# Performance work log

Hardware: AMD Instinct MI355X
Metric: run time of the kernel (lower is better)

## Reference

```python
import jax, jax.numpy as jnp
from jax import lax
import numpy as np

NHEADS = 8

def _conv_block2d(x, w, b):
    y = lax.conv_general_dilated(x, w, (2, 2), [(1, 1), (1, 1)],
                                 dimension_numbers=('NCHW', 'OIHW', 'NCHW'))
    return jax.nn.gelu(y + b[None, :, None, None])

def _conv_block3d(x, w, b):
    y = lax.conv_general_dilated(x, w, (2, 2, 2), [(1, 1)] * 3,
                                 dimension_numbers=('NCDHW', 'OIDHW', 'NCDHW'))
    return jax.nn.gelu(y + b[None, :, None, None, None])

def _layernorm(x, g, b, eps=1e-5):
    mu = x.mean(-1, keepdims=True)
    var = x.var(-1, keepdims=True)
    return (x - mu) / jnp.sqrt(var + eps) * g + b

def _neighborhood_attn(x, g, bln, qkv_w, qkv_b, proj_w, proj_b, dw=5, hw=7, ww=7):
    # x: [B, C, D, H, W]; 3D neighborhood attention, window (dw,hw,ww), zero-pad + mask
    B, C, D, H, W = x.shape
    h, hd = NHEADS, C // NHEADS
    xt = jnp.transpose(x, (0, 2, 3, 4, 1))               # [B,D,H,W,C]
    y = _layernorm(xt, g, bln)
    qkv = y @ qkv_w + qkv_b                               # [B,D,H,W,3C]
    qkv = qkv.reshape(B, D, H, W, 3, h, hd)
    qkv = jnp.transpose(qkv, (4, 0, 5, 6, 1, 2, 3))       # [3,B,h,hd,D,H,W]
    q, k, v = qkv[0] * (hd ** -0.5), qkv[1], qkv[2]
    pz, py, px = dw // 2, hw // 2, ww // 2
    pad = ((0, 0), (0, 0), (0, 0), (pz, pz), (py, py), (px, px))
    kp, vp = jnp.pad(k, pad), jnp.pad(v, pad)
    valid = jnp.pad(jnp.ones((D, H, W), x.dtype), ((pz, pz), (py, py), (px, px)))
    offs = jnp.stack(jnp.meshgrid(jnp.arange(dw), jnp.arange(hw), jnp.arange(ww), indexing='ij'), -1).reshape(-1, 3)

    def score_step(_, o):
        ks = lax.dynamic_slice(kp, (0, 0, 0, o[0], o[1], o[2]), (B, h, hd, D, H, W))
        m = lax.dynamic_slice(valid, (o[0], o[1], o[2]), (D, H, W))
        return None, ((q * ks).sum(2), m)

    _, (scores, masks) = lax.scan(score_step, None, offs)  # [245,B,h,D,H,W],[245,D,H,W]
    neg = jnp.finfo(scores.dtype).min
    scores = jnp.where(masks[:, None, None] > 0, scores, neg)
    probs = jax.nn.softmax(scores, axis=0)

    def out_step(acc, xs):
        o, p = xs
        vs = lax.dynamic_slice(vp, (0, 0, 0, o[0], o[1], o[2]), (B, h, hd, D, H, W))
        return acc + p[:, :, None] * vs, None

    out0 = jnp.zeros((B, h, hd, D, H, W), x.dtype)
    out, _ = lax.scan(out_step, out0, (offs, probs))
    out = jnp.transpose(out, (0, 3, 4, 5, 1, 2)).reshape(B, D, H, W, C)
    out = out @ proj_w + proj_b
    return x + jnp.transpose(out, (0, 4, 1, 2, 3))

def setup_inputs() -> dict:
    key = jax.random.key(0)
    ks = jax.random.split(key, 16)
    rn = lambda i, shp, s: jax.random.normal(ks[i], shp, jnp.float32) * s
    return {
        'x_2d': rn(0, (1, 8, 256, 512), 1.0),
        'x_3d': rn(1, (1, 5, 24, 256, 512), 1.0),
        'sw0': rn(2, (128, 8, 3, 3), 0.02), 'sb0': jnp.zeros((128,), jnp.float32),
        'sw1': rn(3, (256, 128, 3, 3), 0.02), 'sb1': jnp.zeros((256,), jnp.float32),
        'sw2': rn(4, (512, 256, 3, 3), 0.02), 'sb2': jnp.zeros((512,), jnp.float32),
        'pw0': rn(5, (128, 5, 3, 3, 3), 0.02), 'pb0': jnp.zeros((128,), jnp.float32),
        'pw1': rn(6, (256, 128, 3, 3, 3), 0.02), 'pb1': jnp.zeros((256,), jnp.float32),
        'pw2': rn(7, (512, 256, 3, 3, 3), 0.02), 'pb2': jnp.zeros((512,), jnp.float32),
        'lat_w': rn(8, (512, 512, 1, 1, 1), 0.02), 'lat_b': jnp.zeros((512,), jnp.float32),
        'ln_g': jnp.ones((3, 512), jnp.float32), 'ln_b': jnp.zeros((3, 512), jnp.float32),
        'qkv_w': rn(9, (3, 512, 1536), 0.02), 'qkv_b': jnp.zeros((3, 1536), jnp.float32),
        'proj_w': rn(10, (3, 512, 512), 0.02), 'proj_b': jnp.zeros((3, 512), jnp.float32),
    }

def reference(x_2d, x_3d, sw0, sb0, sw1, sb1, sw2, sb2,
              pw0, pb0, pw1, pb1, pw2, pb2, lat_w, lat_b,
              ln_g, ln_b, qkv_w, qkv_b, proj_w, proj_b):
    s = x_2d
    for w_, b_ in ((sw0, sb0), (sw1, sb1), (sw2, sb2)):
        s = _conv_block2d(s, w_, b_)
    p = x_3d
    for w_, b_ in ((pw0, pb0), (pw1, pb1), (pw2, pb2)):
        p = _conv_block3d(p, w_, b_)
    feats = jnp.concatenate([p, s[:, :, None]], axis=2)   # [B,512,D/8+1,H/8,W/8]
    lat = lax.conv_general_dilated(feats, lat_w, (1, 1, 1), 'VALID',
                                   dimension_numbers=('NCDHW', 'OIDHW', 'NCDHW'))
    lat = lat + lat_b[None, :, None, None, None]
    for i in range(3):
        lat = _neighborhood_attn(lat, ln_g[i], ln_b[i], qkv_w[i], qkv_b[i], proj_w[i], proj_b[i])
    return lat
```

## Files before the change

kernel.cpp:

```cpp
#include <hip/hip_runtime.h>
#include <hip/hip_bf16.h>
#include <math.h>

typedef __hip_bfloat16 bf16;
typedef __attribute__((ext_vector_type(8))) short s8v;
typedef __attribute__((ext_vector_type(4))) float f4v;

__device__ __forceinline__ float ldf(const float* p) { return *p; }
__device__ __forceinline__ float ldf(const bf16* p) { return __bfloat162float(*p); }
__device__ __forceinline__ void stf(float* p, float v) { *p = v; }
__device__ __forceinline__ void stf(bf16* p, float v) { *p = __float2bfloat16(v); }

__device__ __forceinline__ float gelu_tanh(float x) {
    float x3 = x * x * x;
    return 0.5f * x * (1.f + tanhf(0.7978845608028654f * (x + 0.044715f * x3)));
}
__device__ __forceinline__ unsigned short bfbits(float x) {
    bf16 t = __float2bfloat16(x);
    return *(unsigned short*)&t;
}

__device__ __forceinline__ void gload16(const bf16* g, bf16* l)
{
    __builtin_amdgcn_global_load_lds(
        (const __attribute__((address_space(1))) unsigned int*)g,
        (__attribute__((address_space(3))) unsigned int*)l,
        16, 0, 0);
}

__global__ __launch_bounds__(256) void fillcol_k(uint4* __restrict__ p, int nrows,
                                                 int strideGran, int granPerRow)
{
    int i = blockIdx.x * 256 + threadIdx.x;
    int row = i / granPerRow, g = i - row * granPerRow;
    if (row < nrows) p[(size_t)row * strideGran + g] = uint4{0u, 0u, 0u, 0u};
}

__global__ __launch_bounds__(256) void tcast_k(const float* __restrict__ in,
                                               bf16* __restrict__ out, int R, int C)
{
    __shared__ float t[64][65];
    int r0 = blockIdx.x * 64, c0 = blockIdx.y * 64;
    for (int i = threadIdx.x; i < 4096; i += 256) {
        int rr = i >> 6, cc = i & 63;
        int r = r0 + rr, c = c0 + cc;
        t[rr][cc] = (c < C) ? in[(size_t)r * C + c] : 0.f;
    }
    __syncthreads();
    for (int i = threadIdx.x; i < 4096; i += 256) {
        int cc = i >> 6, rr = i & 63;
        int r = r0 + rr, c = c0 + cc;
        if (c < C)
            out[(size_t)c * R + r] = __float2bfloat16(t[rr][cc]);
    }
}

__global__ __launch_bounds__(256) void w1prep_k(const float* __restrict__ w, bf16* __restrict__ o,
                                                int OC, int nic, int ntap, int Kp)
{
    int i = blockIdx.x * 256 + threadIdx.x;
    if (i >= OC * Kp) return;
    int oc = i / Kp, k = i - oc * Kp;
    float v = 0.f;
    if (k < nic * ntap) {
        int tap = k / nic, ic = k - tap * nic;
        v = w[((size_t)oc * nic + ic) * ntap + tap];
    }
    o[i] = __float2bfloat16(v);
}

__global__ __launch_bounds__(256) void cast_k(const float* __restrict__ w, bf16* __restrict__ o, int n)
{
    int i = blockIdx.x * 256 + threadIdx.x;
    if (i < n) o[i] = __float2bfloat16(w[i]);
}

__global__ __launch_bounds__(256) void im2col3d_k(const float* __restrict__ x, bf16* __restrict__ A, int od0)
{
    int gid = blockIdx.x * 256 + threadIdx.x;
    int m = gid / 20, kg = gid - 20 * (gid / 20);
    int ow = m & 255, rowid = m >> 8;
    int oh = rowid & 127, od = od0 + (rowid >> 7);
    int iz0 = 2 * od - 1, iy0 = 2 * oh - 1, ix0 = 2 * ow - 1;
    union { uint4 u; unsigned short h[8]; } pk;
#pragma unroll
    for (int j = 0; j < 8; j++) {
        int k = kg * 8 + j;
        float v = 0.f;
        if (k < 135) {
            int tap = k / 5, ic = k - tap * 5;
            int kz = tap / 9, r = tap - kz * 9;
            int ky = r / 3, kx = r - ky * 3;
            int iz = iz0 + kz, iy = iy0 + ky, ix = ix0 + kx;
            if ((unsigned)iz < 24u && (unsigned)iy < 256u && (unsigned)ix < 512u)
                v = x[(((size_t)ic * 24 + iz) * 256 + iy) * 512 + ix];
        }
        pk.h[j] = bfbits(v);
    }
    *(uint4*)&A[(size_t)m * 160 + kg * 8] = pk.u;
}

__global__ __launch_bounds__(256) void im2col2d_k(const float* __restrict__ x, bf16* __restrict__ A)
{
    int gid = blockIdx.x * 256 + threadIdx.x;
    int m = gid / 12, kg = gid - 12 * (gid / 12);
    int ow = m & 255, oh = m >> 8;
    int iy0 = 2 * oh - 1, ix0 = 2 * ow - 1;
    union { uint4 u; unsigned short h[8]; } pk;
#pragma unroll
    for (int j = 0; j < 8; j++) {
        int k = kg * 8 + j;
        float v = 0.f;
        if (k < 72) {
            int tap = k >> 3, ic = k & 7;
            int ky = tap / 3, kx = tap - ky * 3;
            int iy = iy0 + ky, ix = ix0 + kx;
            if ((unsigned)iy < 256u && (unsigned)ix < 512u)
                v = x[((size_t)ic * 256 + iy) * 512 + ix];
        }
        pk.h[j] = bfbits(v);
    }
    *(uint4*)&A[(size_t)m * 96 + kg * 8] = pk.u;
}

__global__ __launch_bounds__(256) void conv1_gemm(
    const bf16* __restrict__ A, const bf16* __restrict__ W, const float* __restrict__ bias,
    bf16* __restrict__ out, int M, int Kp, int rowOff)
{
    __shared__ __align__(16) bf16 As[128 * 32];
    __shared__ __align__(16) bf16 Bs[128 * 32];
    int tid = threadIdx.x;
    int m0 = blockIdx.x * 128;
    int wave = tid >> 6, lane = tid & 63;
    int wb = tid & 192;
    int wm = (wave >> 1) * 64, wn = (wave & 1) * 64;
    int lm = lane & 15, lq = lane >> 4;
    f4v acc[4][4];
#pragma unroll
    for (int i = 0; i < 4; i++)
#pragma unroll
        for (int j = 0; j < 4; j++) acc[i][j] = f4v{0.f, 0.f, 0.f, 0.f};
    for (int k0 = 0; k0 < Kp; k0 += 32) {
        __syncthreads();
#pragma unroll
        for (int c = 0; c < 2; c++) {
            int i = c * 256 + tid;
            int row = i >> 2, kq = i & 3;
            gload16(&A[(size_t)(m0 + row) * Kp + k0 + kq * 8], &As[(c * 256 + wb) * 8]);
            gload16(&W[(size_t)row * Kp + k0 + kq * 8], &Bs[(c * 256 + wb) * 8]);
        }
        __syncthreads();
        s8v af[4], bfr[4];
#pragma unroll
        for (int mi = 0; mi < 4; mi++) af[mi] = *(const s8v*)&As[(wm + mi * 16 + lm) * 32 + lq * 8];
#pragma unroll
        for (int ni = 0; ni < 4; ni++) bfr[ni] = *(const s8v*)&Bs[(wn + ni * 16 + lm) * 32 + lq * 8];
#pragma unroll
        for (int mi = 0; mi < 4; mi++)
#pragma unroll
            for (int ni = 0; ni < 4; ni++)
                acc[mi][ni] = __builtin_amdgcn_mfma_f32_16x16x32_bf16(af[mi], bfr[ni], acc[mi][ni], 0, 0, 0);
    }
#pragma unroll
    for (int mi = 0; mi < 4; mi++)
#pragma unroll
        for (int ni = 0; ni < 4; ni++)
#pragma unroll
            for (int r = 0; r < 4; r++) {
                int m = m0 + wm + mi * 16 + lq * 4 + r;
                int n = wn + ni * 16 + lm;
                int row = rowOff + (m >> 8), x = m & 255;
                float v = acc[mi][ni][r] + bias[n];
                out[((size_t)row * 258 + 1 + x) * 128 + n] = __float2bfloat16(gelu_tanh(v));
            }
}

template <int BM, int KD>
__global__ __launch_bounds__(256) void conv_mfma2(
    const bf16* __restrict__ in, const bf16* __restrict__ wr, const float* __restrict__ bias,
    bf16* __restrict__ out, int ID, int IH, int IWp, int IC,
    int OH, int OC, int OWS, int outPad, int nx)
{
    constexpr int NI = (BM == 128) ? 4 : 2;
    __shared__ __align__(16) bf16 As[3 * BM * 32];
    __shared__ __align__(16) bf16 Bs[3 * 128 * 32];
    int tid = threadIdx.x;
    int nwg = gridDim.x;
    int bl = blockIdx.x;
    int swz = (bl & 7) * (nwg >> 3) + (bl >> 3);
    int n0 = (swz % nx) * 128;
    int rowid = swz / nx;
    int od = rowid / OH, oh = rowid % OH;
    int wave = tid >> 6, lane = tid & 63;
    int wb = tid & 192;
    int wm = (BM == 128) ? (wave >> 1) * 64 : 0;
    int wn = (BM == 128) ? (wave & 1) * 64 : wave * 32;
    int lm = lane & 15, lq = lane >> 4;
    f4v acc[4][NI];
#pragma unroll
    for (int i = 0; i < 4; i++)
#pragma unroll
        for (int j = 0; j < NI; j++) acc[i][j] = f4v{0.f, 0.f, 0.f, 0.f};

    for (int kz = 0; kz < KD; kz++) {
        int iz = (KD == 3) ? (2 * od + kz - 1) : 0;
        if ((unsigned)iz >= (unsigned)ID) continue;
        for (int ky = 0; ky < 3; ky++) {
            int iy = 2 * oh + ky - 1;
            if ((unsigned)iy >= (unsigned)IH) continue;
            const bf16* inrow = in + ((size_t)iz * IH + iy) * IWp * IC;
            const bf16* wbase = wr + (size_t)((kz * 3 + ky) * 3) * OC * IC;
            for (int kb = 0; kb < IC; kb += 32) {
                __syncthreads();
#pragma unroll
                for (int c = 0; c < (3 * BM) / 64; c++) {
                    int i = c * 256 + tid;
                    int kx = i / (BM * 4);
                    int r = i - kx * (BM * 4);
                    int m = r >> 2, sub = r & 3;
                    gload16(&inrow[(size_t)(2 * m + kx) * IC + kb + sub * 8],
                            &As[(c * 256 + wb) * 8]);
                }
#pragma unroll
                for (int c = 0; c < 6; c++) {
                    int i = c * 256 + tid;
                    int t3 = i >> 9, r = i & 511, n = r >> 2, sub = r & 3;
                    gload16(&wbase[((size_t)t3 * OC + n0 + n) * IC + kb + sub * 8],
                            &Bs[(c * 256 + wb) * 8]);
                }
                __syncthreads();
#pragma unroll
                for (int kx = 0; kx < 3; kx++) {
                    s8v af[4], bfr[NI];
#pragma unroll
                    for (int mi = 0; mi < 4; mi++)
                        af[mi] = *(const s8v*)&As[(kx * BM + wm + mi * 16 + lm) * 32 + lq * 8];
#pragma unroll
                    for (int ni = 0; ni < NI; ni++)
                        bfr[ni] = *(const s8v*)&Bs[(kx * 128 + wn + ni * 16 + lm) * 32 + lq * 8];
#pragma unroll
                    for (int mi = 0; mi < 4; mi++)
#pragma unroll
                        for (int ni = 0; ni < NI; ni++)
                            acc[mi][ni] = __builtin_amdgcn_mfma_f32_16x16x32_bf16(af[mi], bfr[ni], acc[mi][ni], 0, 0, 0);
                }
            }
        }
    }
    size_t orowbase = ((size_t)rowid * OWS + outPad) * OC;
#pragma unroll
    for (int mi = 0; mi < 4; mi++)
#pragma unroll
        for (int ni = 0; ni < NI; ni++)
#pragma unroll
            for (int r = 0; r < 4; r++) {
                int m = wm + mi * 16 + lq * 4 + r;
                int n = n0 + wn + ni * 16 + lm;
                float v = acc[mi][ni][r] + bias[n];
                out[orowbase + (size_t)m * OC + n] = __float2bfloat16(gelu_tanh(v));
            }
}

template <typename OutT, int RES, int VT>
__global__ __launch_bounds__(256) void gemm_bt(
    const bf16* __restrict__ A, const bf16* __restrict__ Bt, const float* __restrict__ bias,
    OutT* __restrict__ C, const float* __restrict__ res, bf16* __restrict__ vt,
    int M, int N, int K)
{
    __shared__ __align__(16) bf16 As[128 * 32];
    __shared__ __align__(16) bf16 Bs[128 * 32];
    int tid = threadIdx.x;
    int n0 = blockIdx.x * 128, m0 = blockIdx.y * 128;
    int wave = tid >> 6, lane = tid & 63;
    int wb = tid & 192;
    int wm = (wave >> 1) * 64, wn = (wave & 1) * 64;
    int lm = lane & 15, lq = lane >> 4;
    f4v acc[4][4];
#pragma unroll
    for (int i = 0; i < 4; i++)
#pragma unroll
        for (int j = 0; j < 4; j++) acc[i][j] = f4v{0.f, 0.f, 0.f, 0.f};
    for (int k0 = 0; k0 < K; k0 += 32) {
        __syncthreads();
#pragma unroll
        for (int c = 0; c < 2; c++) {
            int i = c * 256 + tid;
            int row = i >> 2, kq = i & 3;
            gload16(&A[(size_t)(m0 + row) * K + k0 + kq * 8], &As[(c * 256 + wb) * 8]);
            gload16(&Bt[(size_t)(n0 + row) * K + k0 + kq * 8], &Bs[(c * 256 + wb) * 8]);
        }
        __syncthreads();
        s8v af[4], bfr[4];
#pragma unroll
        for (int mi = 0; mi < 4; mi++) af[mi] = *(const s8v*)&As[(wm + mi * 16 + lm) * 32 + lq * 8];
#pragma unroll
        for (int ni = 0; ni < 4; ni++) bfr[ni] = *(const s8v*)&Bs[(wn + ni * 16 + lm) * 32 + lq * 8];
#pragma unroll
        for (int mi = 0; mi < 4; mi++)
#pragma unroll
            for (int ni = 0; ni < 4; ni++)
                acc[mi][ni] = __builtin_amdgcn_mfma_f32_16x16x32_bf16(af[mi], bfr[ni], acc[mi][ni], 0, 0, 0);
    }
#pragma unroll
    for (int mi = 0; mi < 4; mi++)
#pragma unroll
        for (int ni = 0; ni < 4; ni++) {
            int n = n0 + wn + ni * 16 + lm;
            int mbase = m0 + wm + mi * 16 + lq * 4;
            float b = bias[n];
            if (VT && n >= 1024) {
                ushort4 pk;
                pk.x = bfbits(acc[mi][ni][0] + b);
                pk.y = bfbits(acc[mi][ni][1] + b);
                pk.z = bfbits(acc[mi][ni][2] + b);
                pk.w = bfbits(acc[mi][ni][3] + b);
                *(ushort4*)&vt[(size_t)(n - 1024) * 8192 + mbase] = pk;
            }
#pragma unroll
            for (int r = 0; r < 4; r++) {
                int m = mbase + r;
                float v = acc[mi][ni][r] + b;
                if (RES) v += res[(size_t)m * N + n];
                stf(&C[(size_t)m * N + n], v);
            }
        }
}

__global__ __launch_bounds__(256) void ln_k(
    const float* __restrict__ lat, const float* __restrict__ g, const float* __restrict__ b,
    bf16* __restrict__ y)
{
    int tok = blockIdx.x * 4 + (threadIdx.x >> 6);
    int lane = threadIdx.x & 63;
    const float4* row = (const float4*)&lat[(size_t)tok * 512 + lane * 8];
    float4 a = row[0], c = row[1];
    float s = a.x + a.y + a.z + a.w + c.x + c.y + c.z + c.w;
    float ss = a.x * a.x + a.y * a.y + a.z * a.z + a.w * a.w
             + c.x * c.x + c.y * c.y + c.z * c.z + c.w * c.w;
#pragma unroll
    for (int off = 32; off; off >>= 1) {
        s += __shfl_xor(s, off);
        ss += __shfl_xor(ss, off);
    }
    float mu = s * (1.f / 512.f);
    float var = ss * (1.f / 512.f) - mu * mu;
    float rstd = rsqrtf(var + 1e-5f);
    const float4* gp = (const float4*)&g[lane * 8];
    const float4* bp = (const float4*)&b[lane * 8];
    float4 g0 = gp[0], g1 = gp[1], b0 = bp[0], b1 = bp[1];
    union { uint4 u; unsigned short h[8]; } pk;
    pk.h[0] = bfbits((a.x - mu) * rstd * g0.x + b0.x);
    pk.h[1] = bfbits((a.y - mu) * rstd * g0.y + b0.y);
    pk.h[2] = bfbits((a.z - mu) * rstd * g0.z + b0.z);
    pk.h[3] = bfbits((a.w - mu) * rstd * g0.w + b0.w);
    pk.h[4] = bfbits((c.x - mu) * rstd * g1.x + b1.x);
    pk.h[5] = bfbits((c.y - mu) * rstd * g1.y + b1.y);
    pk.h[6] = bfbits((c.z - mu) * rstd * g1.z + b1.z);
    pk.h[7] = bfbits((c.w - mu) * rstd * g1.w + b1.w);
    *(uint4*)&y[(size_t)tok * 512 + lane * 8] = pk.u;
}

__global__ __launch_bounds__(512) void natt_mfma(
    const bf16* __restrict__ qkv, const bf16* __restrict__ vT, bf16* __restrict__ o)
{
    __shared__ __align__(16) char smem[40960];
    float* mlb = (float*)smem;
    float* obuf = (float*)(smem + 8192);
    int tid = threadIdx.x;
    int bx = blockIdx.x;
    int rd = bx >> 5, rh = bx & 31;
    int d = (rd == 0) ? 1 : (rd == 1) ? 2 : (rd == 2) ? 0 : 3;
    int h = (rh < 26) ? (rh + 3) : (rh == 26) ? 2 : (rh == 27) ? 29
          : (rh == 28) ? 1 : (rh == 29) ? 30 : (rh == 30) ? 0 : 31;
    int rowid = d * 32 + h;
    int head = blockIdx.y;
    int rowbase = rowid * 64;
    int hoff = head * 64;
    int wave = tid >> 6, lane = tid & 63;
    int olane = wave & 3, rhalf = wave >> 2;
    int lm = lane & 15, lq = lane >> 4;
    char* qsb = smem;
    bf16* pb = (bf16*)(smem + 8192 + olane * 8192);

    {
        int row = tid >> 3, sub = tid & 7;
        *(uint4*)(qsb + row * 128 + ((sub * 16) ^ ((row & 7) << 4))) =
            *(const uint4*)&qkv[(size_t)(rowbase + row) * 1536 + hoff + sub * 8];
    }
    {
        uint4 z{0u, 0u, 0u, 0u};
        uint4* zp = (uint4*)(smem + 8192);
        zp[tid] = z; zp[tid + 512] = z; zp[tid + 1024] = z; zp[tid + 1536] = z;
    }
    __syncthreads();

    f4v Oa[2][4];
#pragma unroll
    for (int i = 0; i < 2; i++)
#pragma unroll
        for (int j = 0; j < 4; j++) Oa[i][j] = f4v{0.f, 0.f, 0.f, 0.f};
    float mr[2][4], lr[2][4];
#pragma unroll
    for (int i = 0; i < 2; i++)
#pragma unroll
        for (int j = 0; j < 4; j++) { mr[i][j] = -1e30f; lr[i][j] = 0.f; }

    for (int idx = olane; idx < 35; idx += 4) {
        int dz = idx / 7 - 2, dy = idx % 7 - 3;
        int zz = d + dz, yy = h + dy;
        if ((unsigned)zz >= 4u || (unsigned)yy >= 32u) continue;
        int kbase = (zz * 32 + yy) * 64;
        s8v kf[4][2];
#pragma unroll
        for (int ni = 0; ni < 4; ni++)
#pragma unroll
            for (int c = 0; c < 2; c++)
                kf[ni][c] = *(const s8v*)&qkv[(size_t)(kbase + ni * 16 + lm) * 1536 + 512 + hoff + c * 32 + lq * 8];
#pragma unroll
        for (int mj = 0; mj < 2; mj++) {
            int mi = rhalf * 2 + mj;
            int qrow = mi * 16 + lm;
            s8v qc0 = *(const s8v*)(qsb + qrow * 128 + ((lq * 16) ^ ((qrow & 7) << 4)));
            s8v qc1 = *(const s8v*)(qsb + qrow * 128 + ((64 + lq * 16) ^ ((qrow & 7) << 4)));
            f4v s[4];
#pragma unroll
            for (int ni = 0; ni < 4; ni++) s[ni] = f4v{0.f, 0.f, 0.f, 0.f};
            __builtin_amdgcn_s_setprio(1);
#pragma unroll
            for (int ni = 0; ni < 4; ni++)
                s[ni] = __builtin_amdgcn_mfma_f32_16x16x32_bf16(qc0, kf[ni][0], s[ni], 0, 0, 0);
#pragma unroll
            for (int ni = 0; ni < 4; ni++)
                s[ni] = __builtin_amdgcn_mfma_f32_16x16x32_bf16(qc1, kf[ni][1], s[ni], 0, 0, 0);
            __builtin_amdgcn_s_setprio(0);
#pragma unroll
            for (int r = 0; r < 4; r++) {
                int w0 = mi * 16 + lq * 4 + r;
                float s0v = s[0][r], s1v = s[1][r], s2v = s[2][r], s3v = s[3][r];
                int t = w0 + 8 - lm;
                int niq = (t < 0) ? 0 : (t >> 4);
                niq = (niq > 3) ? 3 : niq;
                float vlo = (niq & 1) ? s1v : s0v;
                float vhi = (niq & 1) ? s3v : s2v;
                float v = (niq & 2) ? vhi : vlo;
                int col = (niq << 4) | lm;
                int dlt = col - w0;
                float vv = ((unsigned)(dlt + 3) <= 6u) ? v * 0.125f : -1e30f;
                float rm = vv;
#pragma unroll
                for (int off = 1; off <= 8; off <<= 1)
                    rm = fmaxf(rm, __shfl_xor(rm, off));
                float mo = mr[mj][r];
                float mn = mo;
                if (__any(rm > mo)) {
                    mn = fmaxf(mo, rm);
                    float al = __expf(mo - mn);
                    mr[mj][r] = mn;
                    lr[mj][r] *= al;
#pragma unroll
                    for (int nd = 0; nd < 4; nd++)
                        Oa[mj][nd][r] *= al;
                }
                float p = __expf(vv - mn);
                float rs = p;
#pragma unroll
                for (int off = 1; off <= 8; off <<= 1)
                    rs += __shfl_xor(rs, off);
                lr[mj][r] += rs;
                pb[(w0 << 6) + (col ^ ((w0 & 7) << 3))] = __float2bfloat16(p);
            }
        }
        s8v vf[4][2];
#pragma unroll
        for (int nd = 0; nd < 4; nd++)
#pragma unroll
            for (int c = 0; c < 2; c++)
                vf[nd][c] = *(const s8v*)&vT[(size_t)(hoff + nd * 16 + lm) * 8192 + kbase + c * 32 + lq * 8];
        __asm__ __volatile__("s_waitcnt lgkmcnt(0)" ::: "memory");
        __builtin_amdgcn_sched_barrier(0);
#pragma unroll
        for (int c = 0; c < 2; c++) {
            s8v pf[2];
#pragma unroll
            for (int mj = 0; mj < 2; mj++) {
                int mi = rhalf * 2 + mj;
                pf[mj] = *(const s8v*)&pb[((mi * 16 + lm) << 6) + ((c * 32 + lq * 8) ^ ((lm & 7) << 3))];
            }
            __builtin_amdgcn_s_setprio(1);
#pragma unroll
            for (int mj = 0; mj < 2; mj++)
#pragma unroll
                for (int nd = 0; nd < 4; nd++)
                    Oa[mj][nd] = __builtin_amdgcn_mfma_f32_16x16x32_bf16(pf[mj], vf[nd][c], Oa[mj][nd], 0, 0, 0);
            __builtin_amdgcn_s_setprio(0);
        }
    }
    __syncthreads();
    if (lm == 0) {
#pragma unroll
        for (int mj = 0; mj < 2; mj++)
#pragma unroll
            for (int r = 0; r < 4; r++) {
                int row = (rhalf * 2 + mj) * 16 + lq * 4 + r;
                mlb[olane * 128 + row] = mr[mj][r];
                mlb[olane * 128 + 64 + row] = lr[mj][r];
            }
    }
    __syncthreads();
    for (int wv = 0; wv < 4; wv++) {
        if (olane == wv) {
#pragma unroll
            for (int mj = 0; mj < 2; mj++)
#pragma unroll
                for (int r = 0; r < 4; r++) {
                    int row = (rhalf * 2 + mj) * 16 + lq * 4 + r;
                    float M = fmaxf(fmaxf(mlb[row], mlb[128 + row]),
                                    fmaxf(mlb[256 + row], mlb[384 + row]));
                    float sc = __expf(mr[mj][r] - M);
#pragma unroll
                    for (int nd = 0; nd < 4; nd++) {
                        int ci = row * 65 + nd * 16 + lm;
                        float add = Oa[mj][nd][r] * sc;
                        obuf[ci] = (wv == 0) ? add : (obuf[ci] + add);
                    }
                }
        }
        __syncthreads();
    }
    {
        int row = tid >> 3, cb = (tid & 7) * 8;
        float m0 = mlb[row], m1 = mlb[128 + row], m2 = mlb[256 + row], m3 = mlb[384 + row];
        float M = fmaxf(fmaxf(m0, m1), fmaxf(m2, m3));
        float L = mlb[64 + row] * __expf(m0 - M) + mlb[192 + row] * __expf(m1 - M)
                + mlb[320 + row] * __expf(m2 - M) + mlb[448 + row] * __expf(m3 - M);
        float inv = 1.f / L;
        union { uint4 u; unsigned short hs[8]; } pk;
#pragma unroll
        for (int j = 0; j < 8; j++)
            pk.hs[j] = bfbits(obuf[row * 65 + cb + j] * inv);
        *(uint4*)&o[(size_t)(rowbase + row) * 512 + hoff + cb] = pk.u;
    }
}

__global__ __launch_bounds__(256) void tout_k(const float* __restrict__ lat, float* __restrict__ out)
{
    __shared__ float t[64][65];
    int p0 = blockIdx.x * 64, c0 = blockIdx.y * 64;
    for (int i = threadIdx.x; i < 4096; i += 256) {
        int r = i >> 6, cc = i & 63;
        t[r][cc] = lat[(size_t)(p0 + r) * 512 + c0 + cc];
    }
    __syncthreads();
    for (int i = threadIdx.x; i < 4096; i += 256) {
        int cc = i >> 6, r = i & 63;
        out[(size_t)(c0 + cc) * 8192 + p0 + r] = t[r][cc];
    }
}

extern "C" void kernel_launch(void* const* d_in, const int* in_sizes, int n_in,
                              void* d_out, int out_size, void* d_ws, size_t ws_size,
                              hipStream_t stream)
{
    const float* x2d = (const float*)d_in[0];
    const float* x3d = (const float*)d_in[1];
    const float* sw0 = (const float*)d_in[2];
    const float* sb0 = (const float*)d_in[3];
    const float* sw1 = (const float*)d_in[4];
    const float* sb1 = (const float*)d_in[5];
    const float* sw2 = (const float*)d_in[6];
    const float* sb2 = (const float*)d_in[7];
    const float* pw0 = (const float*)d_in[8];
    const float* pb0 = (const float*)d_in[9];
    const float* pw1 = (const float*)d_in[10];
    const float* pb1 = (const float*)d_in[11];
    const float* pw2 = (const float*)d_in[12];
    const float* pb2 = (const float*)d_in[13];
    const float* latw = (const float*)d_in[14];
    const float* latb = (const float*)d_in[15];
    const float* lng = (const float*)d_in[16];
    const float* lnb = (const float*)d_in[17];
    const float* qkvw = (const float*)d_in[18];
    const float* qkvb = (const float*)d_in[19];
    const float* projw = (const float*)d_in[20];
    const float* projb = (const float*)d_in[21];
    float* outp = (float*)d_out;

    char* ws = (char*)d_ws;
    bf16* p0pad = (bf16*)(ws + 0);
    bf16* wr3d2 = (bf16*)(ws + 101449728ull);
    bf16* wr3d3 = (bf16*)(ws + 103219200ull);
    bf16* wr2d2 = (bf16*)(ws + 110297088ull);
    bf16* wr2d3 = (bf16*)(ws + 110886912ull);
    bf16* qkvt  = (bf16*)(ws + 113246208ull);
    bf16* projt = (bf16*)(ws + 117964800ull);
    bf16* latbf = (bf16*)(ws + 119537664ull);
    bf16* w13d  = (bf16*)(ws + 120061952ull);
    bf16* w12d  = (bf16*)(ws + 120102912ull);
    bf16* p1pad = (bf16*)(ws + 120127488ull);
    bf16* s0pad = (bf16*)(ws + 145686528ull);
    bf16* s1pad = (bf16*)(ws + 154140672ull);
    bf16* featsT= (bf16*)(ws + 158400512ull);
    float* lat  = (float*)(ws + 166789120ull);
    bf16* A3 = (bf16*)(ws + 120127488ull);
    bf16* A2 = (bf16*)(ws + 158400512ull);
    bf16* ybf    = (bf16*)(ws + 0);
    bf16* qkvbuf = (bf16*)(ws + 8388608ull);
    bf16* attno  = (bf16*)(ws + 33554432ull);
    bf16* vT     = (bf16*)(ws + 41943040ull);

    tcast_k<<<dim3(512, 1), 256, 0, stream>>>(pw1, wr3d2, 32768, 27);
    tcast_k<<<dim3(2048, 1), 256, 0, stream>>>(pw2, wr3d3, 131072, 27);
    tcast_k<<<dim3(512, 1), 256, 0, stream>>>(sw1, wr2d2, 32768, 9);
    tcast_k<<<dim3(2048, 1), 256, 0, stream>>>(sw2, wr2d3, 131072, 9);
    for (int r = 0; r < 3; r++) {
        tcast_k<<<dim3(8, 24), 256, 0, stream>>>(qkvw + (size_t)r * 786432, qkvt + (size_t)r * 786432, 512, 1536);
        tcast_k<<<dim3(8, 8), 256, 0, stream>>>(projw + (size_t)r * 262144, projt + (size_t)r * 262144, 512, 512);
    }
    cast_k<<<1024, 256, 0, stream>>>(latw, latbf, 262144);
    w1prep_k<<<80, 256, 0, stream>>>(pw0, w13d, 128, 5, 27, 160);
    w1prep_k<<<48, 256, 0, stream>>>(sw0, w12d, 128, 8, 9, 96);

    fillcol_k<<<96, 256, 0, stream>>>((uint4*)p0pad, 1536, 4128, 16);

    im2col3d_k<<<15360, 256, 0, stream>>>(x3d, A3, 0);
    conv1_gemm<<<1536, 256, 0, stream>>>(A3, w13d, pb0, p0pad, 196608, 160, 0);
    im2col3d_k<<<15360, 256, 0, stream>>>(x3d, A3, 6);
    conv1_gemm<<<1536, 256, 0, stream>>>(A3, w13d, pb0, p0pad, 196608, 160, 768);

    fillcol_k<<<48, 256, 0, stream>>>((uint4*)p1pad, 384, 4160, 32);
    fillcol_k<<<8, 256, 0, stream>>>((uint4*)s0pad, 128, 4128, 16);
    fillcol_k<<<8, 256, 0, stream>>>((uint4*)s1pad, 64, 4160, 32);
    im2col2d_k<<<1536, 256, 0, stream>>>(x2d, A2);
    conv1_gemm<<<256, 256, 0, stream>>>(A2, w12d, sb0, s0pad, 32768, 96, 0);

    conv_mfma2<128, 1><<<dim3(128), 256, 0, stream>>>(s0pad, wr2d2, sb1, s1pad, 1, 128, 258, 128, 64, 256, 130, 1, 2);
    conv_mfma2<64, 1><<<dim3(128), 256, 0, stream>>>(s1pad, wr2d3, sb2, featsT + (size_t)6144 * 512, 1, 64, 130, 256, 32, 512, 64, 0, 4);
    conv_mfma2<128, 3><<<dim3(768), 256, 0, stream>>>(p0pad, wr3d2, pb1, p1pad, 12, 128, 258, 128, 64, 256, 130, 1, 2);
    conv_mfma2<64, 3><<<dim3(384), 256, 0, stream>>>(p1pad, wr3d3, pb2, featsT, 6, 64, 130, 256, 32, 512, 64, 0, 4);

    gemm_bt<float, 0, 0><<<dim3(4, 64), 256, 0, stream>>>(featsT, latbf, latb, lat, nullptr, nullptr, 8192, 512, 512);

    for (int r = 0; r < 3; r++) {
        ln_k<<<2048, 256, 0, stream>>>(lat, lng + r * 512, lnb + r * 512, ybf);
        gemm_bt<bf16, 0, 1><<<dim3(12, 64), 256, 0, stream>>>(ybf, qkvt + (size_t)r * 786432, qkvb + r * 1536,
                                                              qkvbuf, nullptr, vT, 8192, 1536, 512);
        natt_mfma<<<dim3(128, 8), 512, 0, stream>>>(qkvbuf, vT, attno);
        gemm_bt<float, 1, 0><<<dim3(4, 64), 256, 0, stream>>>(attno, projt + (size_t)r * 262144, projb + r * 512,
                                                              lat, lat, nullptr, 8192, 512, 512);
    }

    tout_k<<<dim3(128, 8), 256, 0, stream>>>(lat, outp);
}
```

Measured before the change: 1.234 ms.

## Double-buffer LDS tiles in conv and GEMM kernels to overlap loads with MFMA

Adds a second shared-memory buffer to the implicit-GEMM conv kernel and the bt GEMM kernel. The next K-slice (or next valid kz/ky panel) is issued with global_load_lds into the alternate buffer before the MFMAs run on the current one. This removes one barrier per iteration and hides global-load latency behind compute. In exchange LDS use doubles, which may lower occupancy, and the conv loop gains a more complex panel iterator.

```diff
diff --git a/kernel.cpp b/kernel.cpp
--- a/kernel.cpp
+++ b/kernel.cpp
@@ -182,8 +182,10 @@
     int OH, int OC, int OWS, int outPad, int nx)
 {
     constexpr int NI = (BM == 128) ? 4 : 2;
-    __shared__ __align__(16) bf16 As[3 * BM * 32];
-    __shared__ __align__(16) bf16 Bs[3 * 128 * 32];
+    constexpr int ASZ = 3 * BM * 32;
+    constexpr int BSZ = 3 * 128 * 32;
+    __shared__ __align__(16) bf16 As[2 * ASZ];
+    __shared__ __align__(16) bf16 Bs[2 * BSZ];
     int tid = threadIdx.x;
     int nwg = gridDim.x;
     int bl = blockIdx.x;
@@ -202,50 +204,72 @@
 #pragma unroll
         for (int j = 0; j < NI; j++) acc[i][j] = f4v{0.f, 0.f, 0.f, 0.f};
 
-    for (int kz = 0; kz < KD; kz++) {
-        int iz = (KD == 3) ? (2 * od + kz - 1) : 0;
-        if ((unsigned)iz >= (unsigned)ID) continue;
-        for (int ky = 0; ky < 3; ky++) {
-            int iy = 2 * oh + ky - 1;
-            if ((unsigned)iy >= (unsigned)IH) continue;
-            const bf16* inrow = in + ((size_t)iz * IH + iy) * IWp * IC;
-            const bf16* wbase = wr + (size_t)((kz * 3 + ky) * 3) * OC * IC;
-            for (int kb = 0; kb < IC; kb += 32) {
-                __syncthreads();
-#pragma unroll
-                for (int c = 0; c < (3 * BM) / 64; c++) {
-                    int i = c * 256 + tid;
-                    int kx = i / (BM * 4);
-                    int r = i - kx * (BM * 4);
-                    int m = r >> 2, sub = r & 3;
-                    gload16(&inrow[(size_t)(2 * m + kx) * IC + kb + sub * 8],
-                            &As[(c * 256 + wb) * 8]);
-                }
-#pragma unroll
-                for (int c = 0; c < 6; c++) {
-                    int i = c * 256 + tid;
-                    int t3 = i >> 9, r = i & 511, n = r >> 2, sub = r & 3;
-                    gload16(&wbase[((size_t)t3 * OC + n0 + n) * IC + kb + sub * 8],
-                            &Bs[(c * 256 + wb) * 8]);
-                }
-                __syncthreads();
-#pragma unroll
-                for (int kx = 0; kx < 3; kx++) {
-                    s8v af[4], bfr[NI];
-#pragma unroll
-                    for (int mi = 0; mi < 4; mi++)
-                        af[mi] = *(const s8v*)&As[(kx * BM + wm + mi * 16 + lm) * 32 + lq * 8];
-#pragma unroll
-                    for (int ni = 0; ni < NI; ni++)
-                        bfr[ni] = *(const s8v*)&Bs[(kx * 128 + wn + ni * 16 + lm) * 32 + lq * 8];
-#pragma unroll
-                    for (int mi = 0; mi < 4; mi++)
-#pragma unroll
-                        for (int ni = 0; ni < NI; ni++)
-                            acc[mi][ni] = __builtin_amdgcn_mfma_f32_16x16x32_bf16(af[mi], bfr[ni], acc[mi][ni], 0, 0, 0);
-                }
-            }
-        }
+    auto panelOK = [&](int pz, int py) -> bool {
+        int iz = (KD == 3) ? (2 * od + pz - 1) : 0;
+        int iy = 2 * oh + py - 1;
+        return (unsigned)iz < (unsigned)ID && (unsigned)iy < (unsigned)IH;
+    };
+    auto nextPanel = [&](int& pz, int& py) -> bool {
+        for (;;) {
+            py++;
+            if (py == 3) { py = 0; pz++; }
+            if (pz >= KD) return false;
+            if (panelOK(pz, py)) return true;
+        }
+    };
+    auto stage = [&](int pz, int py, int pk, int buf) {
+        int iz = (KD == 3) ? (2 * od + pz - 1) : 0;
+        int iy = 2 * oh + py - 1;
+        const bf16* inrow = in + ((size_t)iz * IH + iy) * IWp * IC;
+        const bf16* wbase = wr + (size_t)((pz * 3 + py) * 3) * OC * IC;
+        bf16* Ad = As + buf * ASZ;
+        bf16* Bd = Bs + buf * BSZ;
+#pragma unroll
+        for (int c = 0; c < (3 * BM) / 64; c++) {
+            int i = c * 256 + tid;
+            int kx = i / (BM * 4);
+            int r = i - kx * (BM * 4);
+            int m = r >> 2, sub = r & 3;
+            gload16(&inrow[(size_t)(2 * m + kx) * IC + pk + sub * 8], &Ad[(c * 256 + wb) * 8]);
+        }
+#pragma unroll
+        for (int c = 0; c < 6; c++) {
+            int i = c * 256 + tid;
+            int t3 = i >> 9, r = i & 511, n = r >> 2, sub = r & 3;
+            gload16(&wbase[((size_t)t3 * OC + n0 + n) * IC + pk + sub * 8], &Bd[(c * 256 + wb) * 8]);
+        }
+    };
+
+    int kz = 0, ky = -1, kb = 0;
+    nextPanel(kz, ky);
+    stage(kz, ky, kb, 0);
+    __syncthreads();
+    int cur = 0;
+    bool run = true;
+    while (run) {
+        int nkz = kz, nky = ky, nkb = kb + 32;
+        bool hn = true;
+        if (nkb >= IC) { nkb = 0; hn = nextPanel(nkz, nky); }
+        if (hn) stage(nkz, nky, nkb, cur ^ 1);
+        const bf16* Ab = As + cur * ASZ;
+        const bf16* Bb = Bs + cur * BSZ;
+#pragma unroll
+        for (int kx = 0; kx < 3; kx++) {
+            s8v af[4], bfr[NI];
+#pragma unroll
+            for (int mi = 0; mi < 4; mi++)
+                af[mi] = *(const s8v*)&Ab[(kx * BM + wm + mi * 16 + lm) * 32 + lq * 8];
+#pragma unroll
+            for (int ni = 0; ni < NI; ni++)
+                bfr[ni] = *(const s8v*)&Bb[(kx * 128 + wn + ni * 16 + lm) * 32 + lq * 8];
+#pragma unroll
+            for (int mi = 0; mi < 4; mi++)
+#pragma unroll
+                for (int ni = 0; ni < NI; ni++)
+                    acc[mi][ni] = __builtin_amdgcn_mfma_f32_16x16x32_bf16(af[mi], bfr[ni], acc[mi][ni], 0, 0, 0);
+        }
+        __syncthreads();
+        cur ^= 1; kz = nkz; ky = nky; kb = nkb; run = hn;
     }
     size_t orowbase = ((size_t)rowid * OWS + outPad) * OC;
 #pragma unroll
@@ -267,8 +291,8 @@
     OutT* __restrict__ C, const float* __restrict__ res, bf16* __restrict__ vt,
     int M, int N, int K)
 {
-    __shared__ __align__(16) bf16 As[128 * 32];
-    __shared__ __align__(16) bf16 Bs[128 * 32];
+    __shared__ __align__(16) bf16 As[2 * 128 * 32];
+    __shared__ __align__(16) bf16 Bs[2 * 128 * 32];
     int tid = threadIdx.x;
     int n0 = blockIdx.x * 128, m0 = blockIdx.y * 128;
     int wave = tid >> 6, lane = tid & 63;
@@ -280,26 +304,34 @@
     for (int i = 0; i < 4; i++)
 #pragma unroll
         for (int j = 0; j < 4; j++) acc[i][j] = f4v{0.f, 0.f, 0.f, 0.f};
-    for (int k0 = 0; k0 < K; k0 += 32) {
-        __syncthreads();
+    auto stage = [&](int k0, int buf) {
 #pragma unroll
         for (int c = 0; c < 2; c++) {
             int i = c * 256 + tid;
             int row = i >> 2, kq = i & 3;
-            gload16(&A[(size_t)(m0 + row) * K + k0 + kq * 8], &As[(c * 256 + wb) * 8]);
-            gload16(&Bt[(size_t)(n0 + row) * K + k0 + kq * 8], &Bs[(c * 256 + wb) * 8]);
-        }
-        __syncthreads();
+            gload16(&A[(size_t)(m0 + row) * K + k0 + kq * 8], &As[buf * 4096 + (c * 256 + wb) * 8]);
+            gload16(&Bt[(size_t)(n0 + row) * K + k0 + kq * 8], &Bs[buf * 4096 + (c * 256 + wb) * 8]);
+        }
+    };
+    stage(0, 0);
+    __syncthreads();
+    int cur = 0;
+    for (int k0 = 0; k0 < K; k0 += 32) {
+        if (k0 + 32 < K) stage(k0 + 32, cur ^ 1);
+        const bf16* Ab = As + cur * 4096;
+        const bf16* Bb = Bs + cur * 4096;
         s8v af[4], bfr[4];
 #pragma unroll
-        for (int mi = 0; mi < 4; mi++) af[mi] = *(const s8v*)&As[(wm + mi * 16 + lm) * 32 + lq * 8];
-#pragma unroll
-        for (int ni = 0; ni < 4; ni++) bfr[ni] = *(const s8v*)&Bs[(wn + ni * 16 + lm) * 32 + lq * 8];
+        for (int mi = 0; mi < 4; mi++) af[mi] = *(const s8v*)&Ab[(wm + mi * 16 + lm) * 32 + lq * 8];
+#pragma unroll
+        for (int ni = 0; ni < 4; ni++) bfr[ni] = *(const s8v*)&Bb[(wn + ni * 16 + lm) * 32 + lq * 8];
 #pragma unroll
         for (int mi = 0; mi < 4; mi++)
 #pragma unroll
             for (int ni = 0; ni < 4; ni++)
                 acc[mi][ni] = __builtin_amdgcn_mfma_f32_16x16x32_bf16(af[mi], bfr[ni], acc[mi][ni], 0, 0, 0);
+        __syncthreads();
+        cur ^= 1;
     }
 #pragma unroll
     for (int mi = 0; mi < 4; mi++)
```

Result: slower. 1.291 ms (+4.7%).
